# Performance work log

Hardware: AMD Instinct MI355X
Metric: run time of the kernel (lower is better)

The kernel has to match this reference:

```python
import jax, jax.numpy as jnp
import numpy as np

P, NH, KEEP, TOPK = 16, 8, 0.25, 2


def _sincos_1d(embed_dim, pos):
    omega = np.arange(embed_dim // 2, dtype=np.float64)
    omega /= embed_dim / 2.0
    omega = 1.0 / 10000 ** omega
    out = np.einsum('m,d->md', pos.reshape(-1), omega)
    return np.concatenate([np.sin(out), np.cos(out)], axis=1)


def _sincos_2d(embed_dim, gh, gw):
    grid_h = np.arange(gh, dtype=np.float32)
    grid_w = np.arange(gw, dtype=np.float32)
    grid = np.stack(np.meshgrid(grid_w, grid_h), axis=0).reshape(2, -1)
    emb_h = _sincos_1d(embed_dim // 2, grid[0])  # matches original (uses grid[0])
    emb_w = _sincos_1d(embed_dim // 2, grid[1])
    return np.concatenate([emb_h, emb_w], axis=1).astype(np.float32)


def _ln(x, w, b):
    m = x.mean(-1, keepdims=True)
    v = jnp.mean((x - m) ** 2, axis=-1, keepdims=True)
    return (x - m) * jax.lax.rsqrt(v + 1e-5) * w + b


def _mha(q, kv, in_w, in_b, out_w, out_b, nh):
    D = q.shape[-1]
    dh = D // nh
    wq, wk, wv = jnp.split(in_w, 3, 0)
    bq, bk, bv = jnp.split(in_b, 3, 0)
    qq = (q @ wq.T + bq).reshape(q.shape[0], q.shape[1], nh, dh)
    kk = (kv @ wk.T + bk).reshape(kv.shape[0], kv.shape[1], nh, dh)
    vv = (kv @ wv.T + bv).reshape(kv.shape[0], kv.shape[1], nh, dh)
    att = jax.nn.softmax(jnp.einsum('bqhd,bkhd->bhqk', qq, kk) / jnp.sqrt(jnp.asarray(dh, qq.dtype)), -1)
    o = jnp.einsum('bhqk,bkhd->bqhd', att, vv).reshape(q.shape)
    return o @ out_w.T + out_b


def _moe(x, rw, rb, w1, b1, w2, b2):
    E = w1.shape[0]
    probs = jax.nn.softmax(jnp.einsum('btd,ed->bte', x, rw) + rb, -1)
    tv, ti = jax.lax.top_k(probs, TOPK)
    tw = jax.nn.softmax(tv, -1)
    comb = jnp.sum(jax.nn.one_hot(ti, E, dtype=x.dtype) * tw[..., None], axis=-2)  # [B,T,E]
    y = jnp.zeros_like(x)
    for e in range(E):  # small fixed expert count
        h = jax.nn.gelu(jnp.einsum('btd,fd->btf', x, w1[e]) + b1[e], approximate=False)
        o = jnp.einsum('btf,df->btd', h, w2[e]) + b2[e]
        y = y + comb[..., e:e + 1] * o
    return y


def reference(images, type_ids, noise, conv_w, conv_b, latents, type_emb,
              ca_in_w, ca_in_b, ca_out_w, ca_out_b, ca_ln_w, ca_ln_b,
              blk_in_w, blk_in_b, blk_out_w, blk_out_b,
              blk_ln1_w, blk_ln1_b, blk_ln2_w, blk_ln2_b,
              router_w, router_b, e_w1, e_b1, e_w2, e_b2):
    B, _, Hi, Wi = images.shape
    D = conv_w.shape[0]
    x = jax.lax.conv_general_dilated(images, conv_w, (P, P), 'VALID',
                                     dimension_numbers=('NCHW', 'OIHW', 'NCHW'))
    x = x + conv_b[None, :, None, None]
    gh, gw = Hi // P, Wi // P
    patches = x.reshape(B, D, gh * gw).transpose(0, 2, 1)  # [B,N,D]
    patches = patches + jnp.asarray(_sincos_2d(D, gh, gw))[None] + type_emb[type_ids][:, None, :]
    n = patches.shape[1]
    n_vis = max(1, int(n * KEEP))
    ids_shuffle = jnp.argsort(noise, axis=1)
    ids_keep = ids_shuffle[:, :n_vis]
    ids_mask = ids_shuffle[:, n_vis:]
    visible = jnp.take_along_axis(patches, ids_keep[..., None], axis=1)
    lat = jnp.broadcast_to(latents[None], (B,) + latents.shape)
    lat = _ln(lat + _mha(lat, visible, ca_in_w, ca_in_b, ca_out_w, ca_out_b, NH), ca_ln_w, ca_ln_b)
    L = blk_in_w.shape[0]
    for l in range(L):
        lat = _ln(lat + _mha(lat, lat, blk_in_w[l], blk_in_b[l], blk_out_w[l], blk_out_b[l], NH),
                  blk_ln1_w[l], blk_ln1_b[l])
        lat = _ln(lat + _moe(lat, router_w[l], router_b[l], e_w1[l], e_b1[l], e_w2[l], e_b2[l]),
                  blk_ln2_w[l], blk_ln2_b[l])
    return lat, ids_keep, ids_mask


def setup_inputs():
    key = jax.random.key(0)
    B, D, E, L, V = 4, 768, 8, 6, 1000
    ks = iter(jax.random.split(key, 32))

    def nrm(shape, s=0.02):
        return jax.random.normal(next(ks), shape, jnp.float32) * s

    return {
        'images': jax.random.normal(next(ks), (B, 3, 224, 224), jnp.float32),
        'type_ids': jax.random.randint(next(ks), (B,), 0, V),
        'noise': jax.random.uniform(next(ks), (B, 196), jnp.float32),
        'conv_w': nrm((D, 3, P, P)), 'conv_b': jnp.zeros((D,), jnp.float32),
        'latents': jax.random.normal(next(ks), (256, D), jnp.float32),
        'type_emb': nrm((V, D)),
        'ca_in_w': nrm((3 * D, D)), 'ca_in_b': jnp.zeros((3 * D,), jnp.float32),
        'ca_out_w': nrm((D, D)), 'ca_out_b': jnp.zeros((D,), jnp.float32),
        'ca_ln_w': jnp.ones((D,), jnp.float32), 'ca_ln_b': jnp.zeros((D,), jnp.float32),
        'blk_in_w': nrm((L, 3 * D, D)), 'blk_in_b': jnp.zeros((L, 3 * D), jnp.float32),
        'blk_out_w': nrm((L, D, D)), 'blk_out_b': jnp.zeros((L, D), jnp.float32),
        'blk_ln1_w': jnp.ones((L, D), jnp.float32), 'blk_ln1_b': jnp.zeros((L, D), jnp.float32),
        'blk_ln2_w': jnp.ones((L, D), jnp.float32), 'blk_ln2_b': jnp.zeros((L, D), jnp.float32),
        'router_w': nrm((L, E, D)), 'router_b': jnp.zeros((L, E), jnp.float32),
        'e_w1': nrm((L, E, 2 * D, D)), 'e_b1': jnp.zeros((L, E, 2 * D), jnp.float32),
        'e_w2': nrm((L, E, D, 2 * D)), 'e_b2': jnp.zeros((L, E, D), jnp.float32),
    }
```

## Files before the change

### kernel.cpp

```cpp
#include <hip/hip_runtime.h>
#include <math.h>


namespace {

typedef unsigned short u16;
constexpr int Dm  = 768;
constexpr int ML  = 256;
constexpr int BB  = 4;
constexpr int NP  = 196;
constexpr int NV  = 49;
constexpr int NE  = 8;
constexpr int FH_ = 1536;
constexpr int NL  = 6;
constexpr int NT  = 1024;

typedef __attribute__((ext_vector_type(8))) short bf16x8;
typedef __attribute__((ext_vector_type(4))) float f32x4;

__device__ __forceinline__ u16 f2bf(float f){
  union { float f; unsigned u; } v; v.f = f;
  unsigned r = v.u + 0x7fffu + ((v.u >> 16) & 1u);
  return (u16)(r >> 16);
}
__device__ __forceinline__ void pack8(const float4& a, const float4& b, bf16x8& w){
  w[0]=(short)f2bf(a.x); w[1]=(short)f2bf(a.y); w[2]=(short)f2bf(a.z); w[3]=(short)f2bf(a.w);
  w[4]=(short)f2bf(b.x); w[5]=(short)f2bf(b.y); w[6]=(short)f2bf(b.z); w[7]=(short)f2bf(b.w);
}
__device__ __forceinline__ void gload16(const void* g, void* l){
  __builtin_amdgcn_global_load_lds(
      (const __attribute__((address_space(1))) unsigned int*)g,
      (__attribute__((address_space(3))) unsigned int*)l, 16, 0, 0);
}

__device__ __forceinline__ float blk_sum(float v, float* sh){
#pragma unroll
  for (int off = 32; off; off >>= 1) v += __shfl_xor(v, off);
  int wid = threadIdx.x >> 6;
  if ((threadIdx.x & 63) == 0) sh[wid] = v;
  __syncthreads();
  v = sh[0] + sh[1] + sh[2] + sh[3];
  __syncthreads();
  return v;
}

__global__ __launch_bounds__(256) void prologue_k(
    const float* __restrict__ noise, int* __restrict__ ids,
    float* __restrict__ out_keep, float* __restrict__ out_mask,
    const float* __restrict__ images, u16* __restrict__ viscol,
    const float* __restrict__ s0, const float* __restrict__ s1,
    const float* __restrict__ s2, const float* __restrict__ s3,
    const float* __restrict__ s4, const float* __restrict__ s5,
    u16* __restrict__ d0, u16* __restrict__ d1, u16* __restrict__ d2,
    u16* __restrict__ d3, u16* __restrict__ d4, u16* __restrict__ d5)
{
  int bx = blockIdx.x, tid = threadIdx.x;
  __shared__ float shv[NP];
  __shared__ int shord[NP];
  if (bx < 4){
    int b = bx;
    if (tid < NP) shv[tid] = noise[b * NP + tid];
    __syncthreads();
    if (tid < NP){
      float x = shv[tid];
      int rank = 0;
      for (int j = 0; j < NP; j++){
        float y = shv[j];
        rank += (y < x) || (y == x && j < tid);
      }
      shord[rank] = tid;
    }
    __syncthreads();
    if (tid < NP){
      int id = shord[tid];
      ids[b * NP + tid] = id;
      if (tid < NV) out_keep[b * NV + tid] = (float)id;
      else          out_mask[b * (NP - NV) + (tid - NV)] = (float)id;
    }
    return;
  }
  if (bx < 200){
    int bv = bx - 4;
    int b = bv / NV, vq = bv % NV;
    if (tid < NP) shv[tid] = noise[b * NP + tid];
    __syncthreads();
    if (tid < NP){
      float x = shv[tid];
      int rank = 0;
      for (int j = 0; j < NP; j++){
        float y = shv[j];
        rank += (y < x) || (y == x && j < tid);
      }
      if (rank == vq) shord[0] = tid;
    }
    __syncthreads();
    int pid = shord[0];
    int ph = pid / 14, pw = pid % 14;
    int kh = tid >> 4, kw = tid & 15;
#pragma unroll
    for (int c = 0; c < 3; c++)
      viscol[(long)bv * Dm + c * 256 + tid] =
        f2bf(images[((b * 3 + c) * 224 + ph * 16 + kh) * 224 + pw * 16 + kw]);
    return;
  }
  const long c0 = 147456, c1 = 589824, c2 = 737280, c3 = 3391488, c4 = 4276224, c5 = 4325376;
  long i = (long)(bx - 200) * 256 + tid;
  long stride = (long)(gridDim.x - 200) * 256;
  for (; i < c5; i += stride){
    const float* s; u16* d; long off;
    if      (i < c0){ s = s0; d = d0; off = i; }
    else if (i < c1){ s = s1; d = d1; off = i - c0; }
    else if (i < c2){ s = s2; d = d2; off = i - c1; }
    else if (i < c3){ s = s3; d = d3; off = i - c2; }
    else if (i < c4){ s = s4; d = d4; off = i - c3; }
    else            { s = s5; d = d5; off = i - c4; }
    float4 v = *(const float4*)(s + off * 4);
    ushort4 o;
    o.x = f2bf(v.x); o.y = f2bf(v.y); o.z = f2bf(v.z); o.w = f2bf(v.w);
    *(ushort4*)(d + off * 4) = o;
  }
}

template<int MTILE, int NTILE, bool BF16B, bool MOE, bool GATHER, bool POSTYPE>
__global__ __launch_bounds__(256) void g2_k(
    const u16* __restrict__ A, int lda,
    const void* __restrict__ Bv, int ldb, long bSB,
    const float* __restrict__ bias, long biasE,
    float* __restrict__ Cf, u16* __restrict__ Cb, int ldc,
    int M, int N, int K, int act,
    const int* __restrict__ counts, const int* __restrict__ offsets,
    const int* __restrict__ ptok, int mbPerE,
    const int* __restrict__ ids, const int* __restrict__ type_ids,
    const float* __restrict__ type_emb)
{
  constexpr int AF  = MTILE / 64;
  constexpr int MF  = MTILE / 32;
  constexpr int BFN = NTILE / 64;
  constexpr int NF2 = NTILE / 32;
  constexpr int BR  = (NTILE == 128) ? 4 : 2;
  __shared__ __align__(16) short lsa[2][MTILE * 32];
  __shared__ __align__(16) short lsb[2][NTILE * 32];
  int t = threadIdx.x, lane = t & 63, wid = t >> 6;
  int n0 = blockIdx.x * NTILE;
  int m0, cnt = 0, off = 0;
  const u16* B16 = (const u16*)Bv;
  const float* B32 = (const float*)Bv;
  const float* bb = bias;
  if (MOE){
    int e = blockIdx.y / mbPerE, mb = blockIdx.y - e * mbPerE;
    cnt = counts[e]; m0 = mb * MTILE;
    if (m0 >= cnt) return;
    off = offsets[e];
    if (BF16B) B16 += (long)e * bSB; else B32 += (long)e * bSB;
    bb += (long)e * biasE;
  } else {
    m0 = blockIdx.y * MTILE;
  }

  long aoff[AF];
#pragma unroll
  for (int i = 0; i < AF; i++){
    int idx = i * 256 + t, c = idx / MTILE, r = idx % MTILE;
    int gl = m0 + r;
    long row;
    if (MOE) row = (gl < cnt) ? (GATHER ? (long)ptok[off + gl] : (long)(off + gl))
                              : (GATHER ? (long)ptok[off] : (long)off);
    else     row = (gl < M) ? gl : 0;
    aoff[i] = row * (long)lda + c * 8;
  }
  long boff[BFN];
#pragma unroll
  for (int i = 0; i < BFN; i++) boff[i] = 0;
  int bcol = 0, bkh = 0;
  const float* b32p = nullptr;
  if (BF16B){
#pragma unroll
    for (int i = 0; i < BFN; i++){
      int idx = i * 256 + t, c = idx / NTILE, r = idx % NTILE;
      int gc = n0 + r; if (gc >= N) gc = 0;
      boff[i] = (long)gc * ldb + c * 8;
    }
  } else {
    if (NTILE == 128){ bcol = t >> 1; bkh = (t & 1) << 4; }
    else             { bcol = t >> 2; bkh = (t & 3) << 3; }
    int gc = n0 + bcol; if (gc >= N) gc = N - 1;
    b32p = B32 + (long)gc * ldb + bkh;
  }

  float4 br[BR];
  auto stage = [&](int buf, int k0){
#pragma unroll
    for (int i = 0; i < AF; i++)
      gload16(A + aoff[i] + k0, &lsa[buf][(i * 256 + wid * 64) * 8]);
    if (BF16B){
#pragma unroll
      for (int i = 0; i < BFN; i++)
        gload16(B16 + boff[i] + k0, &lsb[buf][(i * 256 + wid * 64) * 8]);
    } else {
#pragma unroll
      for (int j = 0; j < BR; j++) br[j] = *(const float4*)(b32p + k0 + j * 4);
    }
  };
  auto bwrite = [&](int buf){
    if (!BF16B){
      if (NTILE == 128){
        bf16x8 w0, w1;
        pack8(br[0], br[1], w0); pack8(br[2], br[3], w1);
        int c0 = bkh >> 3;
        *(bf16x8*)&lsb[buf][((c0    ) * 128 + bcol) * 8] = w0;
        *(bf16x8*)&lsb[buf][((c0 + 1) * 128 + bcol) * 8] = w1;
      } else {
        bf16x8 w0;
        pack8(br[0], br[1], w0);
        *(bf16x8*)&lsb[buf][((bkh >> 3) * 64 + bcol) * 8] = w0;
      }
    }
  };

  f32x4 acc[MF][NF2];
#pragma unroll
  for (int m = 0; m < MF; m++)
#pragma unroll
    for (int n = 0; n < NF2; n++) acc[m][n] = (f32x4){0.f,0.f,0.f,0.f};

  int T = K >> 5;
  stage(0, 0);
  bwrite(0);
  __syncthreads();

  int wr = wid >> 1, wc = wid & 1, fr = lane & 15, lk = lane >> 4;
  for (int tt = 0; tt < T; tt++){
    int cur = tt & 1, nxt = cur ^ 1;
    if (tt + 1 < T) stage(nxt, (tt + 1) << 5);
    bf16x8 av[MF], bv[NF2];
#pragma unroll
    for (int m = 0; m < MF; m++)
      av[m] = *(const bf16x8*)&lsa[cur][(lk * MTILE + wr * (MTILE / 2) + m * 16 + fr) * 8];
#pragma unroll
    for (int n = 0; n < NF2; n++)
      bv[n] = *(const bf16x8*)&lsb[cur][(lk * NTILE + wc * (NTILE / 2) + n * 16 + fr) * 8];
#pragma unroll
    for (int m = 0; m < MF; m++)
#pragma unroll
      for (int n = 0; n < NF2; n++)
        acc[m][n] = __builtin_amdgcn_mfma_f32_16x16x32_bf16(av[m], bv[n], acc[m][n], 0, 0, 0);
    if (tt + 1 < T) bwrite(nxt);
    __syncthreads();
  }

#pragma unroll
  for (int m = 0; m < MF; m++)
#pragma unroll
  for (int i = 0; i < 4; i++){
    int rl = m0 + wr * (MTILE / 2) + m * 16 + lk * 4 + i;
    bool ok = MOE ? (rl < cnt) : (rl < M);
    if (!ok) continue;
    long grow = MOE ? (long)(off + rl) : (long)rl;
    int pph = 0, ppw = 0, pty = 0;
    if (POSTYPE){
      int pb = rl / NV;
      int pid = ids[pb * NP + rl % NV];
      pph = pid / 14; ppw = pid % 14;
      pty = type_ids[pb];
    }
#pragma unroll
    for (int n = 0; n < NF2; n++){
      int col = n0 + wc * (NTILE / 2) + n * 16 + fr;
      if (col >= N) continue;
      float v = acc[m][n][i] + bb[col];
      if (act) v = 0.5f * v * (1.0f + erff(v * 0.70710678118654752f));
      if (POSTYPE){
        int q = col % 192, sect = col / 192;
        float omega = powf(10000.0f, -(float)q / 192.0f);
        float arg = (sect < 2 ? (float)ppw : (float)pph) * omega;
        float pos = ((sect & 1) == 0) ? sinf(arg) : cosf(arg);
        v += pos + type_emb[(long)pty * Dm + col];
      }
      if (Cf) Cf[grow * (long)ldc + col] = v;
      if (Cb) Cb[grow * (long)ldc + col] = f2bf(v);
    }
  }
}

template<int KVCAP>
__global__ __launch_bounds__(256) void flash_k(
    const u16* __restrict__ Qp, int ldq, int qBatchRows,
    const u16* __restrict__ Kp, int ldk,
    const u16* __restrict__ Vp, int ldv, int kvBatchRows,
    int qCol0, int kCol0, int vCol0,
    int kvLen, u16* __restrict__ Ob)
{
  constexpr int NF   = KVCAP / 16;
  constexpr int HALF = (KVCAP > 128) ? 128 : KVCAP;
  constexpr int NHF  = KVCAP / HALF;

  __shared__ __align__(16) char sm[49152];
  short* smQ  = (short*)sm;
  short* smK0 = (short*)(sm + 12288);
  short* smK1 = (short*)(sm + 12288 + 4 * KVCAP * 16);
  short* smP  = (short*)sm;
  short* smVT = (short*)(sm + 64 * HALF * 2);

  int t = threadIdx.x, lane = t & 63, wid = t >> 6;
  int fr = lane & 15, lk = lane >> 4;
  int qt = blockIdx.x, z = blockIdx.y, b = z >> 3, h = z & 7;
  int qRow0 = b * qBatchRows + qt * 64;
  int kvRow0 = b * kvBatchRows;
  int oRow0 = b * 256 + qt * 64;
  int qCol = qCol0 + h * 96, kCol = kCol0 + h * 96, vCol = vCol0 + h * 96;
  int wq0 = wid * 16;

#pragma unroll
  for (int i = 0; i < 3; i++){
    int idx = i * 256 + t, c = idx >> 6, r = idx & 63;
    *(bf16x8*)&smQ[idx * 8] = *(const bf16x8*)&Qp[(long)(qRow0 + r) * ldq + qCol + c * 8];
  }
  auto stageK = [&](int k0c, short* dst){
#pragma unroll
    for (int i = 0; i < (4 * KVCAP) / 256; i++){
      int idx = i * 256 + t, c = idx / KVCAP, col = idx % KVCAP;
      int kv = col < kvLen ? col : kvLen - 1;
      *(bf16x8*)&dst[idx * 8] =
        *(const bf16x8*)&Kp[(long)(kvRow0 + kv) * ldk + kCol + (k0c * 4 + c) * 8];
    }
  };
  stageK(0, smK0);
  __syncthreads();

  f32x4 acc[NF];
#pragma unroll
  for (int n = 0; n < NF; n++) acc[n] = (f32x4){0.f,0.f,0.f,0.f};

  for (int k0c = 0; k0c < 3; k0c++){
    short* curK = (k0c & 1) ? smK1 : smK0;
    if (k0c < 2) stageK(k0c + 1, (k0c & 1) ? smK0 : smK1);
    bf16x8 av = *(const bf16x8*)&smQ[((k0c * 4 + lk) * 64 + wq0 + fr) * 8];
#pragma unroll
    for (int n = 0; n < NF; n++){
      bf16x8 bv = *(const bf16x8*)&curK[(lk * KVCAP + n * 16 + fr) * 8];
      acc[n] = __builtin_amdgcn_mfma_f32_16x16x32_bf16(av, bv, acc[n], 0, 0, 0);
    }
    __syncthreads();
  }

  const float scl = 0.10206207261596577f;
  float rinv[4];
#pragma unroll
  for (int i = 0; i < 4; i++){
    float mx = -3e38f;
#pragma unroll
    for (int n = 0; n < NF; n++){
      float v = acc[n][i] * scl;
      if (n * 16 + fr >= kvLen) v = -3e38f;
      acc[n][i] = v;
      mx = fmaxf(mx, v);
    }
#pragma unroll
    for (int s = 1; s < 16; s <<= 1) mx = fmaxf(mx, __shfl_xor(mx, s));
    float sum = 0.f;
#pragma unroll
    for (int n = 0; n < NF; n++){
      float p = __expf(acc[n][i] - mx);
      acc[n][i] = p;
      sum += p;
    }
#pragma unroll
    for (int s = 1; s < 16; s <<= 1) sum += __shfl_xor(sum, s);
    rinv[i] = 1.0f / sum;
  }

  f32x4 acco[6];
#pragma unroll
  for (int n = 0; n < 6; n++) acco[n] = (f32x4){0.f,0.f,0.f,0.f};

  for (int hf = 0; hf < NHF; hf++){
    if (hf) __syncthreads();
#pragma unroll
    for (int np = 0; np < HALF / 16; np++){
      int n = hf * (HALF / 16) + np;
#pragma unroll
      for (int i = 0; i < 4; i++){
        int row = wq0 + lk * 4 + i;
        int cl = np * 16 + fr;
        smP[((cl >> 3) * 64 + row) * 8 + (cl & 7)] = (short)f2bf(acc[n][i]);
      }
    }
    constexpr int G = (HALF * 96 / 8) / 256;
#pragma unroll
    for (int g = 0; g < G; g++){
      int flat = g * 256 + t;
      int kvl = flat / 12, dblk = (flat % 12) * 8;
      int kvg = hf * HALF + kvl;
      int kva = kvg < kvLen ? kvg : kvLen - 1;
      bf16x8 v = *(const bf16x8*)&Vp[(long)(kvRow0 + kva) * ldv + vCol + dblk];
      bool zz = kvg >= kvLen;
#pragma unroll
      for (int j = 0; j < 8; j++)
        smVT[((kvl >> 3) * 96 + dblk + j) * 8 + (kvl & 7)] = zz ? (short)0 : v[j];
    }
    __syncthreads();
#pragma unroll
    for (int kk = 0; kk < HALF / 32; kk++){
      bf16x8 pa = *(const bf16x8*)&smP[((kk * 4 + lk) * 64 + wq0 + fr) * 8];
#pragma unroll
      for (int n = 0; n < 6; n++){
        bf16x8 bv = *(const bf16x8*)&smVT[((kk * 4 + lk) * 96 + n * 16 + fr) * 8];
        acco[n] = __builtin_amdgcn_mfma_f32_16x16x32_bf16(pa, bv, acco[n], 0, 0, 0);
      }
    }
  }

#pragma unroll
  for (int n = 0; n < 6; n++)
#pragma unroll
  for (int i = 0; i < 4; i++){
    int row = oRow0 + wq0 + lk * 4 + i;
    Ob[(long)row * 768 + h * 96 + n * 16 + fr] = f2bf(acco[n][i] * rinv[i]);
  }
}

__global__ __launch_bounds__(256) void add_ln_k(
    const float* __restrict__ X, const float* __restrict__ R, int rMod,
    const float* __restrict__ w, const float* __restrict__ b,
    float* __restrict__ outf, u16* __restrict__ outb)
{
  int row = blockIdx.x;
  int rrow = rMod ? (row % rMod) : row;
  __shared__ float sh[4];
  float x[3];
#pragma unroll
  for (int i = 0; i < 3; i++){
    int d = threadIdx.x + (i << 8);
    x[i] = X[(long)row * Dm + d] + R[(long)rrow * Dm + d];
  }
  float s = blk_sum(x[0] + x[1] + x[2], sh);
  float mean = s * (1.0f / 768.0f);
  float vs = 0.f;
#pragma unroll
  for (int i = 0; i < 3; i++){ float tt = x[i] - mean; vs += tt * tt; }
  vs = blk_sum(vs, sh);
  float rstd = rsqrtf(vs * (1.0f / 768.0f) + 1e-5f);
#pragma unroll
  for (int i = 0; i < 3; i++){
    int d = threadIdx.x + (i << 8);
    float o = (x[i] - mean) * rstd * w[d] + b[d];
    outf[(long)row * Dm + d] = o;
    if (outb) outb[(long)row * Dm + d] = f2bf(o);
  }
}

__global__ __launch_bounds__(256) void router_k(
    const float* __restrict__ lat, const float* __restrict__ rw, const float* __restrict__ rb,
    int* __restrict__ top_idx, float* __restrict__ top_w)
{
  int t = blockIdx.x, tid = threadIdx.x;
  int e = tid >> 5, lane = tid & 31;
  const float* x = lat + (long)t * Dm;
  const float* w = rw + (long)e * Dm;
  float s = 0.f;
  for (int j = 0; j < 24; j++){ int d = lane + 32 * j; s += x[d] * w[d]; }
#pragma unroll
  for (int off = 16; off; off >>= 1) s += __shfl_xor(s, off);
  __shared__ float lg[NE];
  if (lane == 0) lg[e] = s + rb[e];
  __syncthreads();
  if (tid == 0){
    float m = -1e30f;
    for (int i = 0; i < NE; i++) m = fmaxf(m, lg[i]);
    float p[NE]; float se = 0.f;
    for (int i = 0; i < NE; i++){ p[i] = __expf(lg[i] - m); se += p[i]; }
    float inv = 1.0f / se;
    int i0 = 0, i1 = -1; float v0 = -1.f, v1 = -1.f;
    for (int i = 0; i < NE; i++){
      float pi = p[i] * inv;
      if (pi > v0){ v1 = v0; i1 = i0; v0 = pi; i0 = i; }
      else if (pi > v1){ v1 = pi; i1 = i; }
    }
    float w0 = 1.0f / (1.0f + __expf(v1 - v0));
    top_idx[2 * t] = i0; top_idx[2 * t + 1] = i1;
    top_w[2 * t] = w0;   top_w[2 * t + 1] = 1.0f - w0;
  }
}

__global__ __launch_bounds__(256) void scatter_k(
    const int* __restrict__ top_idx, int* __restrict__ counts, int* __restrict__ offsets,
    int* __restrict__ ptok, int* __restrict__ posmap)
{
  __shared__ int cnt[NE], cur[NE];
  int tid = threadIdx.x;
  if (tid < NE) cnt[tid] = 0;
  __syncthreads();
  for (int t = tid; t < NT; t += 256){
    atomicAdd(&cnt[top_idx[2 * t]], 1);
    atomicAdd(&cnt[top_idx[2 * t + 1]], 1);
  }
  __syncthreads();
  if (tid == 0){
    int o = 0;
    for (int e = 0; e < NE; e++){ offsets[e] = o; cur[e] = o; counts[e] = cnt[e]; o += cnt[e]; }
  }
  __syncthreads();
  for (int t = tid; t < NT; t += 256){
#pragma unroll
    for (int sidx = 0; sidx < 2; sidx++){
      int e = top_idx[2 * t + sidx];
      int pos = atomicAdd(&cur[e], 1);
      ptok[pos] = t;
      posmap[2 * t + sidx] = pos;
    }
  }
}

__global__ __launch_bounds__(256) void moe_combine_ln_k(
    const float* __restrict__ OBuf, const int* __restrict__ posmap, const float* __restrict__ topw,
    const float* __restrict__ latin, const float* __restrict__ w, const float* __restrict__ b,
    float* __restrict__ outf, u16* __restrict__ outb)
{
  int t = blockIdx.x;
  int p0 = posmap[2 * t], p1 = posmap[2 * t + 1];
  float w0 = topw[2 * t], w1 = topw[2 * t + 1];
  __shared__ float sh[4];
  float x[3];
#pragma unroll
  for (int i = 0; i < 3; i++){
    int d = threadIdx.x + (i << 8);
    x[i] = w0 * OBuf[(long)p0 * Dm + d] + w1 * OBuf[(long)p1 * Dm + d] + latin[(long)t * Dm + d];
  }
  float s = blk_sum(x[0] + x[1] + x[2], sh);
  float mean = s * (1.0f / 768.0f);
  float vs = 0.f;
#pragma unroll
  for (int i = 0; i < 3; i++){ float tt = x[i] - mean; vs += tt * tt; }
  vs = blk_sum(vs, sh);
  float rstd = rsqrtf(vs * (1.0f / 768.0f) + 1e-5f);
#pragma unroll
  for (int i = 0; i < 3; i++){
    int d = threadIdx.x + (i << 8);
    float o = (x[i] - mean) * rstd * w[d] + b[d];
    outf[(long)t * Dm + d] = o;
    if (outb) outb[(long)t * Dm + d] = f2bf(o);
  }
}

}

extern "C" void kernel_launch(void* const* d_in, const int* in_sizes, int n_in,
                              void* d_out, int out_size, void* d_ws, size_t ws_size,
                              hipStream_t stream)
{
  (void)in_sizes; (void)n_in; (void)out_size; (void)ws_size;
  const float* images    = (const float*)d_in[0];
  const int*   type_ids  = (const int*)d_in[1];
  const float* noise     = (const float*)d_in[2];
  const float* conv_w    = (const float*)d_in[3];
  const float* conv_b    = (const float*)d_in[4];
  const float* latents   = (const float*)d_in[5];
  const float* type_emb  = (const float*)d_in[6];
  const float* ca_in_w   = (const float*)d_in[7];
  const float* ca_in_b   = (const float*)d_in[8];
  const float* ca_out_w  = (const float*)d_in[9];
  const float* ca_out_b  = (const float*)d_in[10];
  const float* ca_ln_w   = (const float*)d_in[11];
  const float* ca_ln_b   = (const float*)d_in[12];
  const float* blk_in_w  = (const float*)d_in[13];
  const float* blk_in_b  = (const float*)d_in[14];
  const float* blk_out_w = (const float*)d_in[15];
  const float* blk_out_b = (const float*)d_in[16];
  const float* blk_ln1_w = (const float*)d_in[17];
  const float* blk_ln1_b = (const float*)d_in[18];
  const float* blk_ln2_w = (const float*)d_in[19];
  const float* blk_ln2_b = (const float*)d_in[20];
  const float* router_w  = (const float*)d_in[21];
  const float* router_b  = (const float*)d_in[22];
  const float* e_w1      = (const float*)d_in[23];
  const float* e_b1      = (const float*)d_in[24];
  const float* e_w2      = (const float*)d_in[25];
  const float* e_b2      = (const float*)d_in[26];

  char* W = (char*)d_ws;
  float* lat   = (float*)(W + 0);
  float* tmp   = (float*)(W + 3145728);
  float* obuf  = (float*)(W + 6291456);
  float* topw  = (float*)(W + 13185024);
  int*   ids      = (int*)(W + 13193216);
  int*   top_idx  = (int*)(W + 13197312);
  int*   posmap   = (int*)(W + 13205504);
  int*   ptok     = (int*)(W + 13213696);
  int*   counts   = (int*)(W + 13221888);
  int*   offsets  = (int*)(W + 13221952);
  u16* lat_bf    = (u16*)(W + 13258752);
  u16* ao_bf     = (u16*)(W + 14831616);
  u16* qkv_bf    = (u16*)(W + 16404480);
  u16* h_bf      = (u16*)(W + 21123072);
  u16* viscol_bf = (u16*)(W + 27414528);
  u16* vis_bf    = (u16*)(W + 27715584);
  u16* qq_bf     = (u16*)(W + 28016640);
  u16* kkvv_bf   = (u16*)(W + 28409856);
  u16* lat0_bf   = (u16*)(W + 29011968);
  u16* convw_bf  = (u16*)(W + 29405184);
  u16* caw_bf    = (u16*)(W + 30584832);
  u16* caow_bf   = (u16*)(W + 34123776);
  u16* blkin_bf  = (u16*)(W + 35303424);
  u16* blkout_bf = (u16*)(W + 56537088);

  float* out      = (float*)d_out;
  float* out_lat  = out;
  float* out_keep = out + (long)NT * Dm;
  float* out_mask = out_keep + BB * NV;

  dim3 blk(256);

  prologue_k<<<2248, blk, 0, stream>>>(
      noise, ids, out_keep, out_mask, images, viscol_bf,
      conv_w, ca_in_w, ca_out_w, blk_in_w, blk_out_w, latents,
      convw_bf, caw_bf, caow_bf, blkin_bf, blkout_bf, lat0_bf);

  g2_k<64,64,true,false,false,true><<<dim3(12, 4), blk, 0, stream>>>(
      viscol_bf, Dm, convw_bf, Dm, 0, conv_b, 0,
      nullptr, vis_bf, Dm, BB * NV, Dm, Dm, 0,
      nullptr, nullptr, nullptr, 1, ids, type_ids, type_emb);

  g2_k<64,64,true,false,false,false><<<dim3(12, 4), blk, 0, stream>>>(
      lat0_bf, Dm, caw_bf, Dm, 0, ca_in_b, 0,
      nullptr, qq_bf, Dm, ML, Dm, Dm, 0,
      nullptr, nullptr, nullptr, 1, nullptr, nullptr, nullptr);
  g2_k<64,64,true,false,false,false><<<dim3(24, 4), blk, 0, stream>>>(
      vis_bf, Dm, caw_bf + 768 * 768, Dm, 0, ca_in_b + 768, 0,
      nullptr, kkvv_bf, 1536, BB * NV, 1536, Dm, 0,
      nullptr, nullptr, nullptr, 1, nullptr, nullptr, nullptr);
  flash_k<64><<<dim3(4, 32), blk, 0, stream>>>(
      qq_bf, Dm, 0, kkvv_bf, 1536, kkvv_bf, 1536, NV, 0, 0, 768, NV, ao_bf);
  g2_k<64,64,true,false,false,false><<<dim3(12, 16), blk, 0, stream>>>(
      ao_bf, Dm, caow_bf, Dm, 0, ca_out_b, 0,
      tmp, nullptr, Dm, NT, Dm, Dm, 0,
      nullptr, nullptr, nullptr, 1, nullptr, nullptr, nullptr);
  add_ln_k<<<NT, blk, 0, stream>>>(tmp, latents, ML, ca_ln_w, ca_ln_b, lat, lat_bf);

  for (int l = 0; l < NL; l++){
    g2_k<64,64,true,false,false,false><<<dim3(36, 16), blk, 0, stream>>>(
        lat_bf, Dm, blkin_bf + (long)l * 2304 * 768, Dm, 0, blk_in_b + (long)l * 2304, 0,
        nullptr, qkv_bf, 2304, NT, 2304, Dm, 0,
        nullptr, nullptr, nullptr, 1, nullptr, nullptr, nullptr);
    flash_k<256><<<dim3(4, 32), blk, 0, stream>>>(
        qkv_bf, 2304, ML, qkv_bf, 2304, qkv_bf, 2304, ML, 0, 768, 1536, ML, ao_bf);
    g2_k<64,64,true,false,false,false><<<dim3(12, 16), blk, 0, stream>>>(
        ao_bf, Dm, blkout_bf + (long)l * 768 * 768, Dm, 0, blk_out_b + (long)l * 768, 0,
        tmp, nullptr, Dm, NT, Dm, Dm, 0,
        nullptr, nullptr, nullptr, 1, nullptr, nullptr, nullptr);
    add_ln_k<<<NT, blk, 0, stream>>>(tmp, lat, 0,
        blk_ln1_w + (long)l * 768, blk_ln1_b + (long)l * 768, lat, lat_bf);
    router_k<<<NT, blk, 0, stream>>>(lat, router_w + (long)l * NE * Dm,
                                     router_b + (long)l * NE, top_idx, topw);
    scatter_k<<<1, blk, 0, stream>>>(top_idx, counts, offsets, ptok, posmap);
    g2_k<64,64,false,true,true,false><<<dim3(24, 128), blk, 0, stream>>>(
        lat_bf, Dm, e_w1 + (long)l * NE * FH_ * Dm, Dm, (long)FH_ * Dm,
        e_b1 + (long)l * NE * FH_, FH_,
        nullptr, h_bf, FH_, 0, FH_, Dm, 1,
        counts, offsets, ptok, 16, nullptr, nullptr, nullptr);
    g2_k<64,64,false,true,false,false><<<dim3(12, 128), blk, 0, stream>>>(
        h_bf, FH_, e_w2 + (long)l * NE * Dm * FH_, FH_, (long)Dm * FH_,
        e_b2 + (long)l * NE * Dm, Dm,
        obuf, nullptr, Dm, 0, Dm, FH_, 0,
        counts, offsets, ptok, 16, nullptr, nullptr, nullptr);
    moe_combine_ln_k<<<NT, blk, 0, stream>>>(obuf, posmap, topw, lat,
        blk_ln2_w + (long)l * 768, blk_ln2_b + (long)l * 768,
        (l == NL - 1) ? out_lat : lat, (l == NL - 1) ? nullptr : lat_bf);
  }
}
```

Baseline: 1.066 ms.

## Fuse MoE token scatter into router via global atomics and fixed-capacity expert slots

Removes the single-block scatter kernel: the router now appends each token directly into a fixed-capacity per-expert slot region with global atomics, and per-layer counters are zeroed once in the prologue. Expert offsets become constant e*CAP, so the workspace is relaid out with larger h and obuf buffers. The MoE GEMM block index is remapped so consecutive blocks cycle across experts, spreading early-exit empty tiles. This saves a serial one-block launch per layer at the cost of global atomic contention and a nondeterministic token order within each expert.

```diff
diff --git a/kernel.cpp b/kernel.cpp
--- a/kernel.cpp
+++ b/kernel.cpp
@@ -14,6 +14,7 @@
 constexpr int FH_ = 1536;
 constexpr int NL  = 6;
 constexpr int NT  = 1024;
+constexpr int CAP = 1024;
 
 typedef __attribute__((ext_vector_type(8))) short bf16x8;
 typedef __attribute__((ext_vector_type(4))) float f32x4;
@@ -52,13 +53,18 @@
     const float* __restrict__ s2, const float* __restrict__ s3,
     const float* __restrict__ s4, const float* __restrict__ s5,
     u16* __restrict__ d0, u16* __restrict__ d1, u16* __restrict__ d2,
-    u16* __restrict__ d3, u16* __restrict__ d4, u16* __restrict__ d5)
+    u16* __restrict__ d3, u16* __restrict__ d4, u16* __restrict__ d5,
+    int* __restrict__ gcnt, int* __restrict__ offsets)
 {
   int bx = blockIdx.x, tid = threadIdx.x;
   __shared__ float shv[NP];
   __shared__ int shord[NP];
   if (bx < 4){
     int b = bx;
+    if (b == 0){
+      if (tid >= 200 && tid < 200 + NL * NE) gcnt[tid - 200] = 0;
+      if (tid >= 248 && tid < 256) offsets[tid - 248] = (tid - 248) * CAP;
+    }
     if (tid < NP) shv[tid] = noise[b * NP + tid];
     __syncthreads();
     if (tid < NP){
@@ -141,20 +147,23 @@
   __shared__ __align__(16) short lsa[2][MTILE * 32];
   __shared__ __align__(16) short lsb[2][NTILE * 32];
   int t = threadIdx.x, lane = t & 63, wid = t >> 6;
-  int n0 = blockIdx.x * NTILE;
-  int m0, cnt = 0, off = 0;
+  int n0, m0, cnt = 0, off = 0;
   const u16* B16 = (const u16*)Bv;
   const float* B32 = (const float*)Bv;
   const float* bb = bias;
   if (MOE){
-    int e = blockIdx.y / mbPerE, mb = blockIdx.y - e * mbPerE;
+    int lin = blockIdx.x + gridDim.x * blockIdx.y;
+    int e = lin & 7, r = lin >> 3;
+    int mb = r & (mbPerE - 1), nblk = r / mbPerE;
     cnt = counts[e]; m0 = mb * MTILE;
+    n0 = nblk * NTILE;
     if (m0 >= cnt) return;
     off = offsets[e];
     if (BF16B) B16 += (long)e * bSB; else B32 += (long)e * bSB;
     bb += (long)e * biasE;
   } else {
     m0 = blockIdx.y * MTILE;
+    n0 = blockIdx.x * NTILE;
   }
 
   long aoff[AF];
@@ -437,7 +446,7 @@
   float mean = s * (1.0f / 768.0f);
   float vs = 0.f;
 #pragma unroll
-  for (int i = 0; i < 3; i++){ float tt = x[i] - mean; vs += tt * tt; }
+  for (int i = 0; i < 3; i++){ float t = x[i] - mean; vs += t * t; }
   vs = blk_sum(vs, sh);
   float rstd = rsqrtf(vs * (1.0f / 768.0f) + 1e-5f);
 #pragma unroll
@@ -451,7 +460,8 @@
 
 __global__ __launch_bounds__(256) void router_k(
     const float* __restrict__ lat, const float* __restrict__ rw, const float* __restrict__ rb,
-    int* __restrict__ top_idx, float* __restrict__ top_w)
+    int* __restrict__ ptok, int* __restrict__ posmap,
+    float* __restrict__ top_w, int* __restrict__ gcnt)
 {
   int t = blockIdx.x, tid = threadIdx.x;
   int e = tid >> 5, lane = tid & 31;
@@ -477,37 +487,13 @@
       else if (pi > v1){ v1 = pi; i1 = i; }
     }
     float w0 = 1.0f / (1.0f + __expf(v1 - v0));
-    top_idx[2 * t] = i0; top_idx[2 * t + 1] = i1;
     top_w[2 * t] = w0;   top_w[2 * t + 1] = 1.0f - w0;
-  }
-}
-
-__global__ __launch_bounds__(256) void scatter_k(
-    const int* __restrict__ top_idx, int* __restrict__ counts, int* __restrict__ offsets,
-    int* __restrict__ ptok, int* __restrict__ posmap)
-{
-  __shared__ int cnt[NE], cur[NE];
-  int tid = threadIdx.x;
-  if (tid < NE) cnt[tid] = 0;
-  __syncthreads();
-  for (int t = tid; t < NT; t += 256){
-    atomicAdd(&cnt[top_idx[2 * t]], 1);
-    atomicAdd(&cnt[top_idx[2 * t + 1]], 1);
-  }
-  __syncthreads();
-  if (tid == 0){
-    int o = 0;
-    for (int e = 0; e < NE; e++){ offsets[e] = o; cur[e] = o; counts[e] = cnt[e]; o += cnt[e]; }
-  }
-  __syncthreads();
-  for (int t = tid; t < NT; t += 256){
-#pragma unroll
-    for (int sidx = 0; sidx < 2; sidx++){
-      int e = top_idx[2 * t + sidx];
-      int pos = atomicAdd(&cur[e], 1);
-      ptok[pos] = t;
-      posmap[2 * t + sidx] = pos;
-    }
+    int pos0 = atomicAdd(&gcnt[i0], 1);
+    ptok[i0 * CAP + pos0] = t;
+    posmap[2 * t] = i0 * CAP + pos0;
+    int pos1 = atomicAdd(&gcnt[i1], 1);
+    ptok[i1 * CAP + pos1] = t;
+    posmap[2 * t + 1] = i1 * CAP + pos1;
   }
 }
 
@@ -580,28 +566,27 @@
   char* W = (char*)d_ws;
   float* lat   = (float*)(W + 0);
   float* tmp   = (float*)(W + 3145728);
-  float* obuf  = (float*)(W + 6291456);
   float* topw  = (float*)(W + 13185024);
   int*   ids      = (int*)(W + 13193216);
-  int*   top_idx  = (int*)(W + 13197312);
   int*   posmap   = (int*)(W + 13205504);
-  int*   ptok     = (int*)(W + 13213696);
-  int*   counts   = (int*)(W + 13221888);
-  int*   offsets  = (int*)(W + 13221952);
-  u16* lat_bf    = (u16*)(W + 13258752);
-  u16* ao_bf     = (u16*)(W + 14831616);
-  u16* qkv_bf    = (u16*)(W + 16404480);
-  u16* h_bf      = (u16*)(W + 21123072);
-  u16* viscol_bf = (u16*)(W + 27414528);
-  u16* vis_bf    = (u16*)(W + 27715584);
-  u16* qq_bf     = (u16*)(W + 28016640);
-  u16* kkvv_bf   = (u16*)(W + 28409856);
-  u16* lat0_bf   = (u16*)(W + 29011968);
-  u16* convw_bf  = (u16*)(W + 29405184);
-  u16* caw_bf    = (u16*)(W + 30584832);
-  u16* caow_bf   = (u16*)(W + 34123776);
-  u16* blkin_bf  = (u16*)(W + 35303424);
-  u16* blkout_bf = (u16*)(W + 56537088);
+  int*   gcnt     = (int*)(W + 13221888);
+  int*   offsets  = (int*)(W + 13222144);
+  int*   ptok     = (int*)(W + 13222400);
+  u16* lat_bf    = (u16*)(W + 13255168);
+  u16* ao_bf     = (u16*)(W + 14828032);
+  u16* qkv_bf    = (u16*)(W + 16400896);
+  u16* viscol_bf = (u16*)(W + 21119488);
+  u16* vis_bf    = (u16*)(W + 21420544);
+  u16* qq_bf     = (u16*)(W + 21721600);
+  u16* kkvv_bf   = (u16*)(W + 22114816);
+  u16* lat0_bf   = (u16*)(W + 22716928);
+  u16* convw_bf  = (u16*)(W + 23110144);
+  u16* caw_bf    = (u16*)(W + 24289792);
+  u16* caow_bf   = (u16*)(W + 27828736);
+  u16* blkin_bf  = (u16*)(W + 29008384);
+  u16* blkout_bf = (u16*)(W + 50242048);
+  u16* h_bf      = (u16*)(W + 57319936);
+  float* obuf    = (float*)(W + 82485760);
 
   float* out      = (float*)d_out;
   float* out_lat  = out;
@@ -613,7 +598,8 @@
   prologue_k<<<2248, blk, 0, stream>>>(
       noise, ids, out_keep, out_mask, images, viscol_bf,
       conv_w, ca_in_w, ca_out_w, blk_in_w, blk_out_w, latents,
-      convw_bf, caw_bf, caow_bf, blkin_bf, blkout_bf, lat0_bf);
+      convw_bf, caw_bf, caow_bf, blkin_bf, blkout_bf, lat0_bf,
+      gcnt, offsets);
 
   g2_k<64,64,true,false,false,true><<<dim3(12, 4), blk, 0, stream>>>(
       viscol_bf, Dm, convw_bf, Dm, 0, conv_b, 0,
@@ -650,18 +636,18 @@
     add_ln_k<<<NT, blk, 0, stream>>>(tmp, lat, 0,
         blk_ln1_w + (long)l * 768, blk_ln1_b + (long)l * 768, lat, lat_bf);
     router_k<<<NT, blk, 0, stream>>>(lat, router_w + (long)l * NE * Dm,
-                                     router_b + (long)l * NE, top_idx, topw);
-    scatter_k<<<1, blk, 0, stream>>>(top_idx, counts, offsets, ptok, posmap);
+                                     router_b + (long)l * NE,
+                                     ptok, posmap, topw, gcnt + l * NE);
     g2_k<64,64,false,true,true,false><<<dim3(24, 128), blk, 0, stream>>>(
         lat_bf, Dm, e_w1 + (long)l * NE * FH_ * Dm, Dm, (long)FH_ * Dm,
         e_b1 + (long)l * NE * FH_, FH_,
         nullptr, h_bf, FH_, 0, FH_, Dm, 1,
-        counts, offsets, ptok, 16, nullptr, nullptr, nullptr);
+        gcnt + l * NE, offsets, ptok, 16, nullptr, nullptr, nullptr);
     g2_k<64,64,false,true,false,false><<<dim3(12, 128), blk, 0, stream>>>(
         h_bf, FH_, e_w2 + (long)l * NE * Dm * FH_, FH_, (long)Dm * FH_,
         e_b2 + (long)l * NE * Dm, Dm,
         obuf, nullptr, Dm, 0, Dm, FH_, 0,
-        counts, offsets, ptok, 16, nullptr, nullptr, nullptr);
+        gcnt + l * NE, offsets, ptok, 16, nullptr, nullptr, nullptr);
     moe_combine_ln_k<<<NT, blk, 0, stream>>>(obuf, posmap, topw, lat,
         blk_ln2_w + (long)l * 768, blk_ln2_b + (long)l * 768,
         (l == NL - 1) ? out_lat : lat, (l == NL - 1) ? nullptr : lat_bf);
```

New measurement: 1.633 ms. 53.1% more time.
